# Optimization experiments

Hardware: AMD Instinct MI355X
Metric: run time of the kernel (lower is better)

## Reference

```python
import jax, jax.numpy as jnp
import numpy as np

N_CLASSES = 64
M_PER_CLASS = 64
EMB = 64
B = N_CLASSES * M_PER_CLASS


def setup_inputs() -> dict:
    key = jax.random.key(0)
    k_emb, = jax.random.split(key, 1)
    embeddings = jax.random.normal(k_emb, (B, EMB), dtype=jnp.float32)
    # labels sorted/grouped by class: class c owns rows [c*M, (c+1)*M)
    target = jnp.repeat(jnp.arange(N_CLASSES, dtype=jnp.int32), M_PER_CLASS)
    bandwidths = jnp.full((N_CLASSES,), 1.0, dtype=jnp.float32)  # init_bandwidth
    w = jnp.float32(10.0)  # init_w
    b = jnp.float32(0.1)   # init_b
    return {"embeddings": embeddings, "bandwidths": bandwidths, "w": w, "b": b, "target": target}


def _kde_softmax_loss(embeddings, bandwidths, w, b, target):
    Bn, _ = embeddings.shape
    N = bandwidths.shape[0]
    M = Bn // N
    # pairwise Euclidean distances (torch.dist p=2)
    sq = jnp.sum(embeddings * embeddings, axis=-1)                      # [B]
    d2 = sq[:, None] + sq[None, :] - 2.0 * (embeddings @ embeddings.T)  # [B,B]
    eye = jnp.eye(Bn, dtype=embeddings.dtype)
    d2 = jnp.maximum(d2, 0.0) + eye  # +eye keeps sqrt grad finite on diagonal
    dist = jnp.sqrt(d2)                                                 # [B,B]
    # columns grouped by class -> [B, N_classes, M_per_class]
    Dg = dist.reshape(Bn, N, M)
    K = jnp.exp(-Dg / (2.0 * bandwidths[None, :, None]))                # [B,N,M]
    self_mask = (1.0 - eye).reshape(Bn, N, M)                           # exclude j == utt
    Ksum = jnp.sum(K * self_mask, axis=-1)                              # [B,N]
    labels = target.astype(jnp.int32)                                   # class of each utt
    # mean over class members excluding self when utt belongs to that class
    counts = jnp.float32(M) - (labels[:, None] == jnp.arange(N)[None, :]).astype(jnp.float32)
    probs = Ksum / counts                                               # [B,N] likelihoods
    probs = w * probs + b                                               # scale_matrix
    logp = jax.nn.log_softmax(probs, axis=-1)
    loss = -jnp.sum(logp[jnp.arange(Bn), labels])                       # softmax_loss sum
    return loss


def reference(embeddings, bandwidths, w, b, target):
    return _kde_softmax_loss(embeddings, bandwidths, w, b, target)
```

## Files before the change

### kernel.cpp

```cpp
#include <hip/hip_runtime.h>

namespace {

constexpr int EMB  = 64;
constexpr int NCLS = 64;
constexpr int BTOT = 4096;
constexpr int S4   = 17;

typedef __bf16 bf16x8 __attribute__((ext_vector_type(8)));
typedef float  f32x4  __attribute__((ext_vector_type(4)));

constexpr size_t EMBH_OFF = 0;
constexpr size_t SQ_OFF   = 524288;
constexpr size_t KS_OFF   = 540672;
constexpr size_t PART_OFF = KS_OFF + (size_t)BTOT * NCLS * 4;
constexpr size_t CNT_OFF  = PART_OFF + 64 * 4;
constexpr size_t WS_NEED  = CNT_OFF + 16;

__device__ __forceinline__ ushort f2bf(float x) {
  uint u = __float_as_uint(x);
  uint r = (u + 0x7fffu + ((u >> 16) & 1u)) >> 16;
  return (ushort)r;
}

__global__ __launch_bounds__(256) void kde_prep(const float* __restrict__ emb,
                                                ushort* __restrict__ embh,
                                                float* __restrict__ sq,
                                                int* __restrict__ cnt) {
  if (blockIdx.x == 0 && threadIdx.x == 0) *cnt = 0;

  const int t = blockIdx.x * 256 + threadIdx.x;
  const float4 v = ((const float4*)emb)[t];
  ushort4 o;
  o.x = f2bf(v.x); o.y = f2bf(v.y); o.z = f2bf(v.z); o.w = f2bf(v.w);
  ((ushort4*)embh)[t] = o;

  float s = v.x * v.x + v.y * v.y + v.z * v.z + v.w * v.w;
  s += __shfl_xor(s, 1);
  s += __shfl_xor(s, 2);
  s += __shfl_xor(s, 4);
  s += __shfl_xor(s, 8);
  if ((threadIdx.x & 15) == 0) sq[t >> 4] = s;
}

__global__ __launch_bounds__(256, 4) void kde_ksum_mfma(const __bf16* __restrict__ embh,
                                                        const float* __restrict__ sq,
                                                        const float* __restrict__ bwv,
                                                        float* __restrict__ ksum) {
  const int tid  = threadIdx.x;
  const int wave = tid >> 6;
  const int lane = tid & 63;
  const int bid  = blockIdx.x;
  const int rowBase = (bid >> 4) * 64;
  const int cls  = (bid & 15) * 4 + wave;
  const int colBase = cls * 64;

  const int lr = lane & 15;
  const int kg = lane >> 4;
  const int koff = kg * 8;

  bf16x8 a0[4], a1[4];
#pragma unroll
  for (int rt = 0; rt < 4; ++rt) {
    const __bf16* ar = embh + (rowBase + rt * 16 + lr) * EMB;
    a0[rt] = *(const bf16x8*)(ar + koff);
    a1[rt] = *(const bf16x8*)(ar + 32 + koff);
  }

  float srv[16];
#pragma unroll
  for (int rt = 0; rt < 4; ++rt) {
    const float4 s4 = *(const float4*)(sq + rowBase + rt * 16 + kg * 4);
    srv[rt * 4 + 0] = s4.x; srv[rt * 4 + 1] = s4.y;
    srv[rt * 4 + 2] = s4.z; srv[rt * 4 + 3] = s4.w;
  }

  const float ninv2bw = -1.0f / (2.0f * bwv[cls]);

  float ksr[16];
#pragma unroll
  for (int v = 0; v < 16; ++v) ksr[v] = 0.f;

#pragma unroll
  for (int ct = 0; ct < 4; ++ct) {
    const int c0 = colBase + ct * 16;
    const __bf16* br = embh + (c0 + lr) * EMB;
    const bf16x8 b0 = *(const bf16x8*)(br + koff);
    const bf16x8 b1 = *(const bf16x8*)(br + 32 + koff);
    const int gc = c0 + lr;
    const float sc = sq[gc];
#pragma unroll
    for (int rt = 0; rt < 4; ++rt) {
      f32x4 acc = {0.f, 0.f, 0.f, 0.f};
      acc = __builtin_amdgcn_mfma_f32_16x16x32_bf16(a0[rt], b0, acc, 0, 0, 0);
      acc = __builtin_amdgcn_mfma_f32_16x16x32_bf16(a1[rt], b1, acc, 0, 0, 0);
#pragma unroll
      for (int i = 0; i < 4; ++i) {
        const int gr = rowBase + rt * 16 + kg * 4 + i;
        float d2 = fmaf(-2.f, acc[i], srv[rt * 4 + i] + sc);
        d2 = fmaxf(d2, 0.f);
        const float Kv = __expf(sqrtf(d2) * ninv2bw);
        ksr[rt * 4 + i] += (gr != gc) ? Kv : 0.f;
      }
    }
  }

#pragma unroll
  for (int m = 1; m < 16; m <<= 1) {
#pragma unroll
    for (int v = 0; v < 16; ++v) ksr[v] += __shfl_xor(ksr[v], m);
  }
  if (lr == 0) {
#pragma unroll
    for (int rt = 0; rt < 4; ++rt)
#pragma unroll
      for (int i = 0; i < 4; ++i)
        ksum[(rowBase + rt * 16 + kg * 4 + i) * NCLS + cls] = ksr[rt * 4 + i];
  }
}

__global__ __launch_bounds__(256) void kde_loss3(const float* __restrict__ ksum,
                                                 const int* __restrict__ target,
                                                 const float* __restrict__ wptr,
                                                 const float* __restrict__ bptr,
                                                 float* __restrict__ partial,
                                                 int* __restrict__ cnt,
                                                 float* __restrict__ out) {
  const int tid = threadIdx.x;
  const int row = blockIdx.x * 64 + (tid >> 2);
  const int q   = tid & 3;
  const float w = wptr[0], b = bptr[0];
  const int label = target[row];
  const float inv64 = 1.0f / 64.0f, inv63 = 1.0f / 63.0f;
  const float4* kr = (const float4*)(ksum + row * NCLS + q * 16);

  float p[16];
#pragma unroll
  for (int j4 = 0; j4 < 4; ++j4) {
    const float4 kv = kr[j4];
    const float kvv[4] = {kv.x, kv.y, kv.z, kv.w};
#pragma unroll
    for (int j = 0; j < 4; ++j) {
      const int c = q * 16 + j4 * 4 + j;
      p[j4 * 4 + j] = w * kvv[j] * ((c == label) ? inv63 : inv64) + b;
    }
  }
  float pmax = -1e30f, plab = -1e30f;
#pragma unroll
  for (int j = 0; j < 16; ++j) {
    pmax = fmaxf(pmax, p[j]);
    plab = fmaxf(plab, (q * 16 + j == label) ? p[j] : -1e30f);
  }
  pmax = fmaxf(pmax, __shfl_xor(pmax, 1));
  pmax = fmaxf(pmax, __shfl_xor(pmax, 2));
  plab = fmaxf(plab, __shfl_xor(plab, 1));
  plab = fmaxf(plab, __shfl_xor(plab, 2));
  float se = 0.f;
#pragma unroll
  for (int j = 0; j < 16; ++j) se += __expf(p[j] - pmax);
  se += __shfl_xor(se, 1);
  se += __shfl_xor(se, 2);
  float loss = 0.25f * (pmax + __logf(se) - plab);

#pragma unroll
  for (int m = 1; m < 64; m <<= 1) loss += __shfl_xor(loss, m);
  __shared__ float wsum[4];
  __shared__ int isLast;
  if ((tid & 63) == 0) wsum[tid >> 6] = loss;
  __syncthreads();
  if (tid == 0) {
    const float s = wsum[0] + wsum[1] + wsum[2] + wsum[3];
    __hip_atomic_store(&partial[blockIdx.x], s, __ATOMIC_RELEASE, __HIP_MEMORY_SCOPE_AGENT);
    const int old = __hip_atomic_fetch_add(cnt, 1, __ATOMIC_ACQ_REL, __HIP_MEMORY_SCOPE_AGENT);
    isLast = (old == 63);
  }
  __syncthreads();
  if (isLast && tid < 64) {
    float v = __hip_atomic_load(&partial[tid], __ATOMIC_ACQUIRE, __HIP_MEMORY_SCOPE_AGENT);
#pragma unroll
    for (int m = 1; m < 64; m <<= 1) v += __shfl_xor(v, m);
    if (tid == 0) *out = v;
  }
}

__device__ __forceinline__ void load_tile64(const float4* __restrict__ g, float4* lds) {
  const int t = threadIdx.x;
#pragma unroll
  for (int p = 0; p < 4; ++p) {
    const int ch  = t + p * 256;
    const int row = ch >> 4, k4 = ch & 15;
    lds[row * S4 + k4] = g[row * 16 + k4];
  }
}

__device__ __forceinline__ void sqnorm64(const float4* lds, float* sq) {
  const int t = threadIdx.x;
  if (t < 64) {
    float s = 0.f;
#pragma unroll
    for (int k4 = 0; k4 < 16; ++k4) {
      const float4 v = lds[t * S4 + k4];
      s += v.x * v.x + v.y * v.y + v.z * v.z + v.w * v.w;
    }
    sq[t] = s;
  }
}

__device__ __forceinline__ void tile_ksum(const float4* rowE, const float4* colE,
                                          const float* sqRow, const float* sqCol,
                                          int rowBase, int colBase, float inv2bw,
                                          float ks[4]) {
  const int t  = threadIdx.x;
  const int cq = t & 15, rq = t >> 4;
  float dot[4][4];
#pragma unroll
  for (int m = 0; m < 4; ++m)
#pragma unroll
    for (int n = 0; n < 4; ++n) dot[m][n] = 0.f;

#pragma unroll 4
  for (int k4 = 0; k4 < 16; ++k4) {
    float4 a[4], bb[4];
#pragma unroll
    for (int m = 0; m < 4; ++m) a[m] = rowE[(rq + 16 * m) * S4 + k4];
#pragma unroll
    for (int n = 0; n < 4; ++n) bb[n] = colE[(cq + 16 * n) * S4 + k4];
#pragma unroll
    for (int m = 0; m < 4; ++m)
#pragma unroll
      for (int n = 0; n < 4; ++n) {
        dot[m][n] += a[m].x * bb[n].x;
        dot[m][n] += a[m].y * bb[n].y;
        dot[m][n] += a[m].z * bb[n].z;
        dot[m][n] += a[m].w * bb[n].w;
      }
  }

#pragma unroll
  for (int m = 0; m < 4; ++m) {
    const int r  = rq + 16 * m;
    const int gr = rowBase + r;
    const float sr = sqRow[r];
    float s = 0.f;
#pragma unroll
    for (int n = 0; n < 4; ++n) {
      const int c  = cq + 16 * n;
      const int gc = colBase + c;
      float d2 = sr + sqCol[c] - 2.f * dot[m][n];
      d2 = fmaxf(d2, 0.f);
      const float K = __expf(-sqrtf(d2) * inv2bw);
      s += (gr != gc) ? K : 0.f;
    }
    s += __shfl_xor(s, 1);
    s += __shfl_xor(s, 2);
    s += __shfl_xor(s, 4);
    s += __shfl_xor(s, 8);
    ks[m] = s;
  }
}

__global__ __launch_bounds__(256) void kde_fused(const float* __restrict__ emb,
                                                 const float* __restrict__ bwv,
                                                 const int* __restrict__ target,
                                                 const float* __restrict__ wptr,
                                                 const float* __restrict__ bptr,
                                                 float* __restrict__ out) {
  __shared__ float4 rowE[64 * S4];
  __shared__ float4 colE[64 * S4];
  __shared__ float sqRow[64], sqCol[64];
  __shared__ float ksumL[64 * NCLS];

  const int rg = blockIdx.x;
  const int rowBase = rg * 64;

  load_tile64((const float4*)(emb + rowBase * EMB), rowE);
  __syncthreads();
  sqnorm64(rowE, sqRow);

  for (int cls = 0; cls < NCLS; ++cls) {
    const int colBase = cls * 64;
    __syncthreads();
    load_tile64((const float4*)(emb + colBase * EMB), colE);
    __syncthreads();
    sqnorm64(colE, sqCol);
    __syncthreads();

    const float inv2bw = 1.0f / (2.0f * bwv[cls]);
    float ks[4];
    tile_ksum(rowE, colE, sqRow, sqCol, rowBase, colBase, inv2bw, ks);
    if ((threadIdx.x & 15) == 0) {
      const int rq = threadIdx.x >> 4;
#pragma unroll
      for (int m = 0; m < 4; ++m)
        ksumL[(rq + 16 * m) * NCLS + cls] = ks[m];
    }
  }
  __syncthreads();

  float loss = 0.f;
  if (threadIdx.x < 64) {
    const int r = threadIdx.x;
    const int row = rowBase + r;
    const int label = target[row];
    const float w = wptr[0], b = bptr[0];
    const float inv64 = 1.0f / 64.0f, inv63 = 1.0f / 63.0f;
    float pmax = -1e30f, plabel = 0.f;
    for (int c = 0; c < NCLS; ++c) {
      const float p = w * ksumL[r * NCLS + c] * ((c == label) ? inv63 : inv64) + b;
      pmax = fmaxf(pmax, p);
      plabel = (c == label) ? p : plabel;
    }
    float se = 0.f;
    for (int c = 0; c < NCLS; ++c) {
      const float p = w * ksumL[r * NCLS + c] * ((c == label) ? inv63 : inv64) + b;
      se += __expf(p - pmax);
    }
    loss = pmax + __logf(se) - plabel;
  }

  __shared__ float red[256];
  red[threadIdx.x] = loss;
  __syncthreads();
  for (int s = 128; s > 0; s >>= 1) {
    if (threadIdx.x < s) red[threadIdx.x] += red[threadIdx.x + s];
    __syncthreads();
  }
  if (threadIdx.x == 0) atomicAdd(out, red[0]);
}

}

extern "C" void kernel_launch(void* const* d_in, const int* in_sizes, int n_in,
                              void* d_out, int out_size, void* d_ws, size_t ws_size,
                              hipStream_t stream) {
  const float* emb    = (const float*)d_in[0];
  const float* bwv    = (const float*)d_in[1];
  const float* wptr   = (const float*)d_in[2];
  const float* bptr   = (const float*)d_in[3];
  const int*   target = (const int*)d_in[4];
  float* out = (float*)d_out;

  if (ws_size >= WS_NEED) {
    ushort* embh    = (ushort*)((char*)d_ws + EMBH_OFF);
    float*  sq      = (float*)((char*)d_ws + SQ_OFF);
    float*  ksum    = (float*)((char*)d_ws + KS_OFF);
    float*  partial = (float*)((char*)d_ws + PART_OFF);
    int*    cnt     = (int*)((char*)d_ws + CNT_OFF);

    kde_prep<<<256, 256, 0, stream>>>(emb, embh, sq, cnt);
    kde_ksum_mfma<<<1024, 256, 0, stream>>>((const __bf16*)embh, sq, bwv, ksum);
    kde_loss3<<<64, 256, 0, stream>>>(ksum, target, wptr, bptr, partial, cnt, out);
  } else {
    hipMemsetAsync(out, 0, sizeof(float), stream);
    kde_fused<<<64, 256, 0, stream>>>(emb, bwv, target, wptr, bptr, out);
  }
}
```

Baseline: 30.98 us.

## Fuse prep, MFMA kernel-sum and loss into one kernel with atomic counters

Removes the separate bf16 conversion/norm kernel by converting fp32 embeddings to bf16 and computing squared norms inline in the MFMA kernel. The per-row-group softmax loss and the final reduction are folded into the same kernel using last-block-done atomic counters, and a memset replaces the in-kernel counter reset. This trades three launches for one memset plus one launch, at the cost of redundant fp32 loads and conversions per block and extra atomic synchronisation.

```diff
diff --git a/kernel.cpp b/kernel.cpp
--- a/kernel.cpp
+++ b/kernel.cpp
@@ -10,70 +10,72 @@
 typedef __bf16 bf16x8 __attribute__((ext_vector_type(8)));
 typedef float  f32x4  __attribute__((ext_vector_type(4)));
 
-constexpr size_t EMBH_OFF = 0;
-constexpr size_t SQ_OFF   = 524288;
-constexpr size_t KS_OFF   = 540672;
-constexpr size_t PART_OFF = KS_OFF + (size_t)BTOT * NCLS * 4;
-constexpr size_t CNT_OFF  = PART_OFF + 64 * 4;
-constexpr size_t WS_NEED  = CNT_OFF + 16;
-
-__device__ __forceinline__ ushort f2bf(float x) {
-  uint u = __float_as_uint(x);
-  uint r = (u + 0x7fffu + ((u >> 16) & 1u)) >> 16;
-  return (ushort)r;
-}
-
-__global__ __launch_bounds__(256) void kde_prep(const float* __restrict__ emb,
-                                                ushort* __restrict__ embh,
-                                                float* __restrict__ sq,
-                                                int* __restrict__ cnt) {
-  if (blockIdx.x == 0 && threadIdx.x == 0) *cnt = 0;
-
-  const int t = blockIdx.x * 256 + threadIdx.x;
-  const float4 v = ((const float4*)emb)[t];
-  ushort4 o;
-  o.x = f2bf(v.x); o.y = f2bf(v.y); o.z = f2bf(v.z); o.w = f2bf(v.w);
-  ((ushort4*)embh)[t] = o;
-
-  float s = v.x * v.x + v.y * v.y + v.z * v.z + v.w * v.w;
-  s += __shfl_xor(s, 1);
-  s += __shfl_xor(s, 2);
-  s += __shfl_xor(s, 4);
-  s += __shfl_xor(s, 8);
-  if ((threadIdx.x & 15) == 0) sq[t >> 4] = s;
-}
-
-__global__ __launch_bounds__(256, 4) void kde_ksum_mfma(const __bf16* __restrict__ embh,
-                                                        const float* __restrict__ sq,
-                                                        const float* __restrict__ bwv,
-                                                        float* __restrict__ ksum) {
+constexpr size_t KS_OFF   = 0;
+constexpr size_t PART_OFF = (size_t)BTOT * NCLS * 4;
+constexpr size_t RGC_OFF  = PART_OFF + 64 * 4;
+constexpr size_t GC_OFF   = RGC_OFF + 64 * 4;
+constexpr size_t CNT_BYTES = 64 * 4 + 4;
+constexpr size_t WS_NEED  = GC_OFF + 16;
+
+__device__ __forceinline__ float cvt16(const float* __restrict__ p,
+                                       bf16x8& lo, bf16x8& hi) {
+  const float4 f0 = *(const float4*)(p);
+  const float4 f1 = *(const float4*)(p + 4);
+  const float4 f2 = *(const float4*)(p + 32);
+  const float4 f3 = *(const float4*)(p + 36);
+  lo[0] = (__bf16)f0.x; lo[1] = (__bf16)f0.y; lo[2] = (__bf16)f0.z; lo[3] = (__bf16)f0.w;
+  lo[4] = (__bf16)f1.x; lo[5] = (__bf16)f1.y; lo[6] = (__bf16)f1.z; lo[7] = (__bf16)f1.w;
+  hi[0] = (__bf16)f2.x; hi[1] = (__bf16)f2.y; hi[2] = (__bf16)f2.z; hi[3] = (__bf16)f2.w;
+  hi[4] = (__bf16)f3.x; hi[5] = (__bf16)f3.y; hi[6] = (__bf16)f3.z; hi[7] = (__bf16)f3.w;
+  float s = f0.x * f0.x + f0.y * f0.y + f0.z * f0.z + f0.w * f0.w;
+  s = fmaf(f1.x, f1.x, s); s = fmaf(f1.y, f1.y, s); s = fmaf(f1.z, f1.z, s); s = fmaf(f1.w, f1.w, s);
+  s = fmaf(f2.x, f2.x, s); s = fmaf(f2.y, f2.y, s); s = fmaf(f2.z, f2.z, s); s = fmaf(f2.w, f2.w, s);
+  s = fmaf(f3.x, f3.x, s); s = fmaf(f3.y, f3.y, s); s = fmaf(f3.z, f3.z, s); s = fmaf(f3.w, f3.w, s);
+  return s;
+}
+
+__global__ __launch_bounds__(256, 4) void kde_all(const float* __restrict__ emb,
+                                                  const float* __restrict__ bwv,
+                                                  const int* __restrict__ target,
+                                                  const float* __restrict__ wptr,
+                                                  const float* __restrict__ bptr,
+                                                  float* __restrict__ ksum,
+                                                  float* __restrict__ partial,
+                                                  unsigned* __restrict__ rgc,
+                                                  unsigned* __restrict__ gcnt,
+                                                  float* __restrict__ out) {
   const int tid  = threadIdx.x;
   const int wave = tid >> 6;
   const int lane = tid & 63;
   const int bid  = blockIdx.x;
-  const int rowBase = (bid >> 4) * 64;
-  const int cls  = (bid & 15) * 4 + wave;
+  const int rg   = bid >> 4;
+  const int cg   = bid & 15;
+  const int rowBase = rg * 64;
+  const int cls  = cg * 4 + wave;
   const int colBase = cls * 64;
 
   const int lr = lane & 15;
   const int kg = lane >> 4;
   const int koff = kg * 8;
 
+  __shared__ int flag;
+  __shared__ float wsum[4];
+
   bf16x8 a0[4], a1[4];
+  float sqr[4];
 #pragma unroll
   for (int rt = 0; rt < 4; ++rt) {
-    const __bf16* ar = embh + (rowBase + rt * 16 + lr) * EMB;
-    a0[rt] = *(const bf16x8*)(ar + koff);
-    a1[rt] = *(const bf16x8*)(ar + 32 + koff);
-  }
-
+    float s = cvt16(emb + (rowBase + rt * 16 + lr) * EMB + koff, a0[rt], a1[rt]);
+    s += __shfl_xor(s, 16);
+    s += __shfl_xor(s, 32);
+    sqr[rt] = s;
+  }
   float srv[16];
 #pragma unroll
-  for (int rt = 0; rt < 4; ++rt) {
-    const float4 s4 = *(const float4*)(sq + rowBase + rt * 16 + kg * 4);
-    srv[rt * 4 + 0] = s4.x; srv[rt * 4 + 1] = s4.y;
-    srv[rt * 4 + 2] = s4.z; srv[rt * 4 + 3] = s4.w;
-  }
+  for (int rt = 0; rt < 4; ++rt)
+#pragma unroll
+    for (int i = 0; i < 4; ++i)
+      srv[rt * 4 + i] = __shfl(sqr[rt], kg * 4 + i);
 
   const float ninv2bw = -1.0f / (2.0f * bwv[cls]);
 
@@ -84,11 +86,11 @@
 #pragma unroll
   for (int ct = 0; ct < 4; ++ct) {
     const int c0 = colBase + ct * 16;
-    const __bf16* br = embh + (c0 + lr) * EMB;
-    const bf16x8 b0 = *(const bf16x8*)(br + koff);
-    const bf16x8 b1 = *(const bf16x8*)(br + 32 + koff);
-    const int gc = c0 + lr;
-    const float sc = sq[gc];
+    bf16x8 b0, b1;
+    float sc = cvt16(emb + (c0 + lr) * EMB + koff, b0, b1);
+    sc += __shfl_xor(sc, 16);
+    sc += __shfl_xor(sc, 32);
+    const int gcidx = c0 + lr;
 #pragma unroll
     for (int rt = 0; rt < 4; ++rt) {
       f32x4 acc = {0.f, 0.f, 0.f, 0.f};
@@ -100,7 +102,7 @@
         float d2 = fmaf(-2.f, acc[i], srv[rt * 4 + i] + sc);
         d2 = fmaxf(d2, 0.f);
         const float Kv = __expf(sqrtf(d2) * ninv2bw);
-        ksr[rt * 4 + i] += (gr != gc) ? Kv : 0.f;
+        ksr[rt * 4 + i] += (gr != gcidx) ? Kv : 0.f;
       }
     }
   }
@@ -117,69 +119,74 @@
       for (int i = 0; i < 4; ++i)
         ksum[(rowBase + rt * 16 + kg * 4 + i) * NCLS + cls] = ksr[rt * 4 + i];
   }
-}
-
-__global__ __launch_bounds__(256) void kde_loss3(const float* __restrict__ ksum,
-                                                 const int* __restrict__ target,
-                                                 const float* __restrict__ wptr,
-                                                 const float* __restrict__ bptr,
-                                                 float* __restrict__ partial,
-                                                 int* __restrict__ cnt,
-                                                 float* __restrict__ out) {
-  const int tid = threadIdx.x;
-  const int row = blockIdx.x * 64 + (tid >> 2);
-  const int q   = tid & 3;
-  const float w = wptr[0], b = bptr[0];
-  const int label = target[row];
-  const float inv64 = 1.0f / 64.0f, inv63 = 1.0f / 63.0f;
-  const float4* kr = (const float4*)(ksum + row * NCLS + q * 16);
-
-  float p[16];
-#pragma unroll
-  for (int j4 = 0; j4 < 4; ++j4) {
-    const float4 kv = kr[j4];
-    const float kvv[4] = {kv.x, kv.y, kv.z, kv.w};
-#pragma unroll
-    for (int j = 0; j < 4; ++j) {
-      const int c = q * 16 + j4 * 4 + j;
-      p[j4 * 4 + j] = w * kvv[j] * ((c == label) ? inv63 : inv64) + b;
-    }
-  }
-  float pmax = -1e30f, plab = -1e30f;
-#pragma unroll
-  for (int j = 0; j < 16; ++j) {
-    pmax = fmaxf(pmax, p[j]);
-    plab = fmaxf(plab, (q * 16 + j == label) ? p[j] : -1e30f);
-  }
-  pmax = fmaxf(pmax, __shfl_xor(pmax, 1));
-  pmax = fmaxf(pmax, __shfl_xor(pmax, 2));
-  plab = fmaxf(plab, __shfl_xor(plab, 1));
-  plab = fmaxf(plab, __shfl_xor(plab, 2));
-  float se = 0.f;
-#pragma unroll
-  for (int j = 0; j < 16; ++j) se += __expf(p[j] - pmax);
-  se += __shfl_xor(se, 1);
-  se += __shfl_xor(se, 2);
-  float loss = 0.25f * (pmax + __logf(se) - plab);
-
-#pragma unroll
-  for (int m = 1; m < 64; m <<= 1) loss += __shfl_xor(loss, m);
-  __shared__ float wsum[4];
-  __shared__ int isLast;
-  if ((tid & 63) == 0) wsum[tid >> 6] = loss;
+
+  __syncthreads();
+  if (tid == 0) {
+    const unsigned old = __hip_atomic_fetch_add(&rgc[rg], 1u, __ATOMIC_ACQ_REL,
+                                                __HIP_MEMORY_SCOPE_AGENT);
+    flag = ((old & 15u) == 15u) ? 1 : 0;
+  }
+  __syncthreads();
+  if (!flag) return;
+
+  {
+    const int row = rowBase + (tid >> 2);
+    const int q   = tid & 3;
+    const float w = wptr[0], b = bptr[0];
+    const int label = target[row];
+    const float inv64 = 1.0f / 64.0f, inv63 = 1.0f / 63.0f;
+    const float4* kr = (const float4*)(ksum + row * NCLS + q * 16);
+
+    float p[16];
+#pragma unroll
+    for (int j4 = 0; j4 < 4; ++j4) {
+      const float4 kv = kr[j4];
+      const float kvv[4] = {kv.x, kv.y, kv.z, kv.w};
+#pragma unroll
+      for (int j = 0; j < 4; ++j) {
+        const int c = q * 16 + j4 * 4 + j;
+        p[j4 * 4 + j] = w * kvv[j] * ((c == label) ? inv63 : inv64) + b;
+      }
+    }
+    float pmax = -1e30f, plab = -1e30f;
+#pragma unroll
+    for (int j = 0; j < 16; ++j) {
+      pmax = fmaxf(pmax, p[j]);
+      plab = fmaxf(plab, (q * 16 + j == label) ? p[j] : -1e30f);
+    }
+    pmax = fmaxf(pmax, __shfl_xor(pmax, 1));
+    pmax = fmaxf(pmax, __shfl_xor(pmax, 2));
+    plab = fmaxf(plab, __shfl_xor(plab, 1));
+    plab = fmaxf(plab, __shfl_xor(plab, 2));
+    float se = 0.f;
+#pragma unroll
+    for (int j = 0; j < 16; ++j) se += __expf(p[j] - pmax);
+    se += __shfl_xor(se, 1);
+    se += __shfl_xor(se, 2);
+    float loss = 0.25f * (pmax + __logf(se) - plab);
+
+#pragma unroll
+    for (int m = 1; m < 64; m <<= 1) loss += __shfl_xor(loss, m);
+    if ((tid & 63) == 0) wsum[tid >> 6] = loss;
+  }
   __syncthreads();
   if (tid == 0) {
     const float s = wsum[0] + wsum[1] + wsum[2] + wsum[3];
-    __hip_atomic_store(&partial[blockIdx.x], s, __ATOMIC_RELEASE, __HIP_MEMORY_SCOPE_AGENT);
-    const int old = __hip_atomic_fetch_add(cnt, 1, __ATOMIC_ACQ_REL, __HIP_MEMORY_SCOPE_AGENT);
-    isLast = (old == 63);
-  }
-  __syncthreads();
-  if (isLast && tid < 64) {
-    float v = __hip_atomic_load(&partial[tid], __ATOMIC_ACQUIRE, __HIP_MEMORY_SCOPE_AGENT);
+    __hip_atomic_store(&partial[rg], s, __ATOMIC_RELEASE, __HIP_MEMORY_SCOPE_AGENT);
+    const unsigned old = __hip_atomic_fetch_add(gcnt, 1u, __ATOMIC_ACQ_REL,
+                                                __HIP_MEMORY_SCOPE_AGENT);
+    flag = ((old & 63u) == 63u) ? 1 : 0;
+  }
+  __syncthreads();
+  if (!flag) return;
+
+  if (tid < 64) {
+    float v = __hip_atomic_load(&partial[tid], __ATOMIC_RELAXED,
+                                __HIP_MEMORY_SCOPE_AGENT);
 #pragma unroll
     for (int m = 1; m < 64; m <<= 1) v += __shfl_xor(v, m);
-    if (tid == 0) *out = v;
+    if (tid == 0)
+      __hip_atomic_store(out, v, __ATOMIC_RELEASE, __HIP_MEMORY_SCOPE_AGENT);
   }
 }
 
@@ -341,15 +348,14 @@
   float* out = (float*)d_out;
 
   if (ws_size >= WS_NEED) {
-    ushort* embh    = (ushort*)((char*)d_ws + EMBH_OFF);
-    float*  sq      = (float*)((char*)d_ws + SQ_OFF);
-    float*  ksum    = (float*)((char*)d_ws + KS_OFF);
-    float*  partial = (float*)((char*)d_ws + PART_OFF);
-    int*    cnt     = (int*)((char*)d_ws + CNT_OFF);
-
-    kde_prep<<<256, 256, 0, stream>>>(emb, embh, sq, cnt);
-    kde_ksum_mfma<<<1024, 256, 0, stream>>>((const __bf16*)embh, sq, bwv, ksum);
-    kde_loss3<<<64, 256, 0, stream>>>(ksum, target, wptr, bptr, partial, cnt, out);
+    float*    ksum    = (float*)((char*)d_ws + KS_OFF);
+    float*    partial = (float*)((char*)d_ws + PART_OFF);
+    unsigned* rgc     = (unsigned*)((char*)d_ws + RGC_OFF);
+    unsigned* gcnt    = (unsigned*)((char*)d_ws + GC_OFF);
+
+    hipMemsetAsync((char*)d_ws + RGC_OFF, 0, CNT_BYTES, stream);
+    kde_all<<<1024, 256, 0, stream>>>(emb, bwv, target, wptr, bptr,
+                                      ksum, partial, rgc, gcnt, out);
   } else {
     hipMemsetAsync(out, 0, sizeof(float), stream);
     kde_fused<<<64, 256, 0, stream>>>(emb, bwv, target, wptr, bptr, out);
```

New measurement: 75.29 us. 143% more time.
